# Kernel optimization log

Measured on AMD Instinct MI355X. Metric: run time of the kernel, lower is better.

## Reference

```python
import jax, jax.numpy as jnp
import numpy as np

LOG_2PI = np.float32(np.log(2.0 * np.pi))
NEG_BIG = np.float32(-9e15)


def setup_inputs() -> dict:
    key = jax.random.key(0)
    ks = jax.random.split(key, 8)
    N, F_in, F_out, H = 8192, 512, 128, 16
    x = jax.random.normal(ks[0], (N, F_in), dtype=jnp.float32)
    adj = jax.random.randint(ks[1], (N, N), 0, 2, dtype=jnp.int32)
    # xavier_uniform-ish init for W (gain 1.414)
    lim = np.float32(1.414 * np.sqrt(6.0 / (F_in + F_out)))
    W = jax.random.uniform(ks[2], (F_in, F_out), jnp.float32, -lim, lim)
    # VariationalAttentionNet params: lin1(2*F_out -> H), lin21/lin22(H -> 1)
    w1 = jax.random.normal(ks[3], (H, 2 * F_out), dtype=jnp.float32) * 0.05
    b1 = jnp.zeros((H,), jnp.float32)
    w21 = jax.random.normal(ks[4], (1, H), dtype=jnp.float32) * 0.05
    b21 = jnp.zeros((1,), jnp.float32)
    w22 = jax.random.normal(ks[5], (1, H), dtype=jnp.float32) * 0.05
    b22 = jnp.zeros((1,), jnp.float32)
    return {"x": x, "adj": adj, "W": W, "w1": w1, "b1": b1,
            "w21": w21, "b21": b21, "w22": w22, "b22": b22}


def reference(x, adj, W, w1, b1, w21, b21, w22, b22):
    # h = x @ W  [N, F_out]
    h = x @ W
    # VariationalAttentionNet(h, h), eval mode: z = mu
    u = jax.nn.relu(jnp.concatenate([h, h], axis=1) @ w1.T + b1)  # [N, H]
    mu = u @ w21.T + b21   # [N, 1]
    lv = u @ w22.T + b22   # [N, 1]
    sigma = jax.nn.softplus(lv)
    z = mu
    # qmp = -(log p(z) - log q(z)); with z = mu, log q(mu) = -log(sigma) - 0.5*log(2pi)
    log_p = jnp.sum(-0.5 * z * z - 0.5 * LOG_2PI)
    log_q = jnp.sum(-jnp.log(sigma) - 0.5 * LOG_2PI)
    qmp = log_q - log_p
    # per-node score z broadcast across row, masked by adjacency, row softmax
    scores = jnp.where(adj > 0, z, NEG_BIG)          # [N, N]
    attention = jax.nn.softmax(scores, axis=1)       # [N, N] (dropout off in eval)
    h_prime = attention @ h                          # [N, F_out]
    return jax.nn.elu(h_prime), qmp
```

## Files before the change

kernel.cpp:

```cpp
#include <hip/hip_runtime.h>

typedef unsigned int u32;
typedef unsigned short u16;

#define NN 8192
#define FIN 512
#define FOUT 128
#define NH 16
#define BK 64
#define BKA 256

typedef float f32x16 __attribute__((ext_vector_type(16)));
typedef __bf16 bf16x8 __attribute__((ext_vector_type(8)));

union PackAB { u32 u[4]; bf16x8 v; };

__device__ __forceinline__ u32 rne_hi(u32 u) {
  return u + (0x7FFFu + ((u >> 16) & 1u));
}
__device__ __forceinline__ u16 f32_to_bf16(float f) {
  return (u16)(rne_hi(__float_as_uint(f)) >> 16);
}

__global__ __launch_bounds__(256) void prep_kernel(
    const float* __restrict__ W, const float* __restrict__ w1,
    u16* __restrict__ WT, float* __restrict__ w1s) {
  int b = blockIdx.x, t = threadIdx.x;
  if (b < 256) {
    int o = b * 256 + t;
    int n = o >> 9, k = o & 511;
    WT[o] = f32_to_bf16(W[k * FOUT + n]);
  } else {
    for (int e = t; e < NH * FOUT; e += 256) {
      int k = e >> 7, f = e & 127;
      w1s[e] = w1[k * 256 + f] + w1[k * 256 + 128 + f];
    }
  }
}

__global__ __launch_bounds__(256, 6) void h_kernel(
    const float* __restrict__ x, const u16* __restrict__ WT,
    float* __restrict__ Hp, int KL) {
  __shared__ u16 aS[32 * BK];
  __shared__ u16 bS[128 * BK];
  int t = threadIdx.x;
  int w = t >> 6, l = t & 63;
  int m = l & 31, kh = l >> 5;
  int tile = blockIdx.x & 255, chunk = blockIdx.x >> 8;
  int i0 = tile * 32, k0 = chunk * KL;

  int arow = t >> 4, acol = (t & 15) * 4;
  int ac = (t & 15) >> 1, ah = t & 1;
  int aoff0 = arow * BK + ((ac ^ (arow & 7)) << 3) + ah * 4;
  int aoff1 = (arow + 16) * BK + ((ac ^ ((arow + 16) & 7)) << 3) + ah * 4;
  const float* ap0 = x + (size_t)(i0 + arow) * FIN + k0 + acol;
  const float* ap1 = ap0 + (size_t)16 * FIN;
  int hr = t >> 3, hc = t & 7;
  const u16* bp0 = WT + (size_t)hr * FIN + k0 + hc * 8;
  int boff[4];
#pragma unroll
  for (int p = 0; p < 4; ++p) {
    int r = hr + 32 * p;
    boff[p] = r * BK + ((hc ^ (r & 7)) << 3);
  }
  int aro = m * BK, am7 = m & 7;
  int nB = w * 32 + m;
  int bro = nB * BK, bm7 = nB & 7;

  f32x16 acc;
#pragma unroll
  for (int r = 0; r < 16; ++r) acc[r] = 0.0f;

  for (int o = 0; o < KL; o += BK) {
    float4 a0 = *(const float4*)ap0;
    float4 a1 = *(const float4*)ap1;
    uint4 h0 = *(const uint4*)bp0;
    uint4 h1 = *(const uint4*)(bp0 + 32 * (size_t)FIN);
    uint4 h2 = *(const uint4*)(bp0 + 64 * (size_t)FIN);
    uint4 h3 = *(const uint4*)(bp0 + 96 * (size_t)FIN);
    ap0 += BK; ap1 += BK; bp0 += BK;
    uint2 w0, w1v;
    w0.x = (rne_hi(__float_as_uint(a0.y)) & 0xFFFF0000u) | (rne_hi(__float_as_uint(a0.x)) >> 16);
    w0.y = (rne_hi(__float_as_uint(a0.w)) & 0xFFFF0000u) | (rne_hi(__float_as_uint(a0.z)) >> 16);
    w1v.x = (rne_hi(__float_as_uint(a1.y)) & 0xFFFF0000u) | (rne_hi(__float_as_uint(a1.x)) >> 16);
    w1v.y = (rne_hi(__float_as_uint(a1.w)) & 0xFFFF0000u) | (rne_hi(__float_as_uint(a1.z)) >> 16);
    *(uint2*)&aS[aoff0] = w0;
    *(uint2*)&aS[aoff1] = w1v;
    *(uint4*)&bS[boff[0]] = h0;
    *(uint4*)&bS[boff[1]] = h1;
    *(uint4*)&bS[boff[2]] = h2;
    *(uint4*)&bS[boff[3]] = h3;
    __syncthreads();
#pragma unroll
    for (int s = 0; s < BK; s += 16) {
      int cA = (s >> 3) + kh;
      PackAB pa, pb;
      pa.v = *(const bf16x8*)&aS[aro + ((cA ^ am7) << 3)];
      pb.v = *(const bf16x8*)&bS[bro + ((cA ^ bm7) << 3)];
      acc = __builtin_amdgcn_mfma_f32_32x32x16_bf16(pa.v, pb.v, acc, 0, 0, 0);
    }
    __syncthreads();
  }
  float* hp = Hp + (size_t)chunk * NN * FOUT;
  int col = w * 32 + m;
#pragma unroll
  for (int r = 0; r < 16; ++r) {
    int row = (r & 3) + 8 * (r >> 2) + 4 * kh;
    hp[(size_t)(i0 + row) * FOUT + col] = acc[r];
  }
}

__global__ __launch_bounds__(256) void reduceH_kernel(
    const float* __restrict__ Hp, int KSH,
    const float* __restrict__ b1, const float* __restrict__ w21,
    const float* __restrict__ b21, const float* __restrict__ w22,
    const float* __restrict__ b22, const float* __restrict__ w1s,
    u16* __restrict__ HTf, float* __restrict__ qpart) {
  __shared__ float hs[32][FOUT + 4];
  __shared__ float w1l[NH][FOUT + 4];
  __shared__ float us[32][NH + 1];
  int t = threadIdx.x;
  int i0 = blockIdx.x * 32;
  float v[16];
  const float* base = Hp + (size_t)i0 * FOUT + t * 16;
#pragma unroll
  for (int e = 0; e < 16; e += 4) {
    float4 x4 = *(const float4*)(base + e);
    v[e] = x4.x; v[e + 1] = x4.y; v[e + 2] = x4.z; v[e + 3] = x4.w;
  }
  for (int c = 1; c < KSH; ++c) {
    const float* p = base + (size_t)c * NN * FOUT;
#pragma unroll
    for (int e = 0; e < 16; e += 4) {
      float4 x4 = *(const float4*)(p + e);
      v[e] += x4.x; v[e + 1] += x4.y; v[e + 2] += x4.z; v[e + 3] += x4.w;
    }
  }
  {
    int row = t >> 3, c0 = (t & 7) * 16;
#pragma unroll
    for (int e = 0; e < 16; ++e) hs[row][c0 + e] = v[e];
  }
  for (int e = t; e < NH * FOUT; e += 256) w1l[e >> 7][e & 127] = w1s[e];
  __syncthreads();
  {
    int n = t & 127, g2 = t >> 7;
#pragma unroll
    for (int gg = 0; gg < 2; ++gg) {
      int g = g2 + 2 * gg;
      int k16 = (i0 >> 4) + (g >> 1), kh = g & 1;
      u32 p[4];
#pragma unroll
      for (int j = 0; j < 4; ++j) {
        u16 lo = f32_to_bf16(hs[g * 8 + 2 * j][n]);
        u16 hi = f32_to_bf16(hs[g * 8 + 2 * j + 1][n]);
        p[j] = (u32)lo | ((u32)hi << 16);
      }
      uint4 st; st.x = p[0]; st.y = p[1]; st.z = p[2]; st.w = p[3];
      size_t off = ((size_t)(k16 * 4 + (n >> 5)) * 64 + kh * 32 + (n & 31)) * 8;
      *(uint4*)(HTf + off) = st;
    }
  }
  {
    int i = t >> 3, p = t & 7;
    float s0 = b1[p], s1 = b1[p + 8];
#pragma unroll 4
    for (int f = 0; f < FOUT; ++f) {
      float hv = hs[i][f];
      s0 = fmaf(hv, w1l[p][f], s0);
      s1 = fmaf(hv, w1l[p + 8][f], s1);
    }
    us[i][p] = fmaxf(s0, 0.0f);
    us[i][p + 8] = fmaxf(s1, 0.0f);
  }
  __syncthreads();
  if (t < 32) {
    float mu = b21[0], lv = b22[0];
#pragma unroll
    for (int k = 0; k < NH; ++k) {
      mu = fmaf(us[t][k], w21[k], mu);
      lv = fmaf(us[t][k], w22[k], lv);
    }
    float sp = fmaxf(lv, 0.0f) + log1pf(expf(-fabsf(lv)));
    float q = 0.5f * mu * mu - logf(sp);
#pragma unroll
    for (int off = 16; off; off >>= 1) q += __shfl_down(q, off);
    if (t == 0) qpart[blockIdx.x] = q;
  }
}

__global__ __launch_bounds__(256, 4) void attn_kernel(
    const int* __restrict__ adj, const u16* __restrict__ HTf,
    float* __restrict__ Sp, u32* __restrict__ degw, int KL) {
  __shared__ u16 aS[2][8192];
  int t = threadIdx.x;
  int w = t >> 6, l = t & 63;
  int m = l & 31, kh = l >> 5;
  int tile = blockIdx.x & 255, chunk = blockIdx.x >> 8;
  int i0 = tile * 32, k0 = chunk * KL;

  int ar = t >> 3, lc = t & 7;
  const int* apb = adj + (size_t)(i0 + ar) * NN + k0 + lc * 4;
  int woff[8];
#pragma unroll
  for (int q = 0; q < 8; ++q)
    woff[q] = (q * 4 + (lc >> 1)) * 256 + ar * 8 + (lc & 1) * 4;
  const u16* bp = HTf + ((size_t)(k0 >> 4) * 256 + (size_t)(w * 64 + l)) * 8;
  int rdo = l * 8;

  f32x16 acc;
#pragma unroll
  for (int r = 0; r < 16; ++r) acc[r] = 0.0f;
  u32 degacc = 0;

  int nslab = KL / BKA;
  int4 aC[8];
#pragma unroll
  for (int q = 0; q < 8; ++q) aC[q] = *(const int4*)(apb + q * 32);
  apb += BKA;
#pragma unroll
  for (int q = 0; q < 8; ++q) {
    u32 p0 = ((u32)aC[q].y << 16) | (u32)aC[q].x;
    u32 p1 = ((u32)aC[q].w << 16) | (u32)aC[q].z;
    degacc += p0 + p1;
    uint2 wv; wv.x = p0 * 0x3F80u; wv.y = p1 * 0x3F80u;
    *(uint2*)&aS[0][woff[q]] = wv;
  }
  if (nslab > 1) {
#pragma unroll
    for (int q = 0; q < 8; ++q) aC[q] = *(const int4*)(apb + q * 32);
    apb += BKA;
  }
  __syncthreads();

  for (int o = 0; o < nslab; ++o) {
    int bsel = o & 1;
    bf16x8 bF[4];
#pragma unroll
    for (int j = 0; j < 4; ++j) bF[j] = *(const bf16x8*)(bp + j * 2048);
#pragma unroll
    for (int k16 = 0; k16 < 16; k16 += 4) {
      bf16x8 bN[4];
      if (k16 + 4 < 16) {
#pragma unroll
        for (int j = 0; j < 4; ++j)
          bN[j] = *(const bf16x8*)(bp + (k16 + 4 + j) * 2048);
      }
#pragma unroll
      for (int j = 0; j < 4; ++j) {
        PackAB pa;
        pa.v = *(const bf16x8*)&aS[bsel][(k16 + j) * 512 + rdo];
        acc = __builtin_amdgcn_mfma_f32_32x32x16_bf16(pa.v, bF[j], acc, 0, 0, 0);
      }
#pragma unroll
      for (int j = 0; j < 4; ++j) bF[j] = bN[j];
    }
    bp += (size_t)16 * 2048;
    if (o + 1 < nslab) {
#pragma unroll
      for (int q = 0; q < 8; ++q) {
        u32 p0 = ((u32)aC[q].y << 16) | (u32)aC[q].x;
        u32 p1 = ((u32)aC[q].w << 16) | (u32)aC[q].z;
        degacc += p0 + p1;
        uint2 wv; wv.x = p0 * 0x3F80u; wv.y = p1 * 0x3F80u;
        *(uint2*)&aS[bsel ^ 1][woff[q]] = wv;
      }
      if (o + 2 < nslab) {
#pragma unroll
        for (int q = 0; q < 8; ++q) aC[q] = *(const int4*)(apb + q * 32);
        apb += BKA;
      }
      __syncthreads();
    }
  }
  u32 d = (degacc & 0xFFFFu) + (degacc >> 16);
  d += __shfl_down(d, 4);
  d += __shfl_down(d, 2);
  d += __shfl_down(d, 1);
  if (lc == 0) degw[chunk * NN + i0 + ar] = d;
  float* sp = Sp + (size_t)chunk * NN * FOUT;
  int col = w * 32 + m;
#pragma unroll
  for (int r = 0; r < 16; ++r) {
    int row = (r & 3) + 8 * (r >> 2) + 4 * kh;
    sp[(size_t)(i0 + row) * FOUT + col] = acc[r];
  }
}

__global__ __launch_bounds__(256) void reduceSq_kernel(
    const float* __restrict__ Sp, const u32* __restrict__ degw,
    const float* __restrict__ qpart, float* __restrict__ out, int KSA) {
  int t = threadIdx.x;
  if (blockIdx.x == 1024) {
    __shared__ float sred[4];
    float v = qpart[t];
#pragma unroll
    for (int off = 32; off; off >>= 1) v += __shfl_down(v, off);
    if ((t & 63) == 0) sred[t >> 6] = v;
    __syncthreads();
    if (t == 0) out[(size_t)NN * FOUT] = sred[0] + sred[1] + sred[2] + sred[3];
    return;
  }
  int idx = (blockIdx.x * 256 + t) * 4;
  int i = idx >> 7;
  u32 deg = 0;
  for (int c = 0; c < KSA; ++c) deg += degw[c * NN + i];
  float4 s = {0.0f, 0.0f, 0.0f, 0.0f};
  for (int c = 0; c < KSA; ++c) {
    float4 v4 = *(const float4*)(Sp + (size_t)c * NN * FOUT + idx);
    s.x += v4.x; s.y += v4.y; s.z += v4.z; s.w += v4.w;
  }
  float rd = deg ? 1.0f / (float)deg : 0.0f;
  float4 o;
  o.x = s.x * rd; o.y = s.y * rd; o.z = s.z * rd; o.w = s.w * rd;
  o.x = o.x > 0.0f ? o.x : expm1f(o.x);
  o.y = o.y > 0.0f ? o.y : expm1f(o.y);
  o.z = o.z > 0.0f ? o.z : expm1f(o.z);
  o.w = o.w > 0.0f ? o.w : expm1f(o.w);
  *(float4*)(out + idx) = o;
}

extern "C" void kernel_launch(void* const* d_in, const int* in_sizes, int n_in,
                              void* d_out, int out_size, void* d_ws, size_t ws_size,
                              hipStream_t stream) {
  (void)in_sizes; (void)n_in; (void)out_size;
  const float* x   = (const float*)d_in[0];
  const int*   adj = (const int*)d_in[1];
  const float* W   = (const float*)d_in[2];
  const float* w1  = (const float*)d_in[3];
  const float* b1  = (const float*)d_in[4];
  const float* w21 = (const float*)d_in[5];
  const float* b21 = (const float*)d_in[6];
  const float* w22 = (const float*)d_in[7];
  const float* b22 = (const float*)d_in[8];
  float* out = (float*)d_out;

  const size_t TILE4 = (size_t)NN * FOUT * 4;
  int KSA = 4, KSH = 4;
  for (;;) {
    size_t need = (size_t)(KSA + KSH) * TILE4
                + (size_t)NN * FOUT * 2
                + (size_t)FOUT * FIN * 2
                + (size_t)KSA * NN * 4
                + NH * FOUT * 4 + 2048;
    if (need <= ws_size || (KSA == 1 && KSH == 1)) break;
    if (KSH > 1) KSH >>= 1; else KSA >>= 1;
  }

  char* ws = (char*)d_ws;
  float* Sp   = (float*)ws;                          ws += (size_t)KSA * TILE4;
  float* Hp   = (float*)ws;                          ws += (size_t)KSH * TILE4;
  u16*   HTf  = (u16*)ws;                            ws += (size_t)NN * FOUT * 2;
  u16*   WT   = (u16*)ws;                            ws += (size_t)FOUT * FIN * 2;
  u32*   degw = (u32*)ws;                            ws += (size_t)KSA * NN * 4;
  float* w1s  = (float*)ws;                          ws += NH * FOUT * 4;
  float* qpart= (float*)ws;

  prep_kernel<<<257, 256, 0, stream>>>(W, w1, WT, w1s);
  h_kernel<<<256 * KSH, 256, 0, stream>>>(x, WT, Hp, FIN / KSH);
  reduceH_kernel<<<256, 256, 0, stream>>>(Hp, KSH, b1, w21, b21, w22, b22, w1s, HTf, qpart);
  attn_kernel<<<256 * KSA, 256, 0, stream>>>(adj, HTf, Sp, degw, NN / KSA);
  reduceSq_kernel<<<1025, 256, 0, stream>>>(Sp, degw, qpart, out, KSA);
}
```

Before: 422.7 us.

## Give each wave private adjacency staging and drop block-wide barriers in attention kernel

The attention kernel now has every wave load and convert its own copy of a 64-column adjacency slab into a per-wave LDS buffer, so the block-wide __syncthreads become wave barriers. The slab depth drops from 256 to 64, the occupancy hint rises from 4 to 5 blocks, and the split-K count for the attention pass doubles to 8. The aim is to remove cross-wave barrier stalls and raise parallelism. The cost is that each adjacency row tile is fetched four times, once per wave, which adds cache and memory traffic, plus more partial-sum output for the reduce pass.

```diff
diff --git a/kernel.cpp b/kernel.cpp
--- a/kernel.cpp
+++ b/kernel.cpp
@@ -8,7 +8,6 @@
 #define FOUT 128
 #define NH 16
 #define BK 64
-#define BKA 256
 
 typedef float f32x16 __attribute__((ext_vector_type(16)));
 typedef __bf16 bf16x8 __attribute__((ext_vector_type(8)));
@@ -189,95 +188,92 @@
   }
 }
 
-__global__ __launch_bounds__(256, 4) void attn_kernel(
+__global__ __launch_bounds__(256, 5) void attn_kernel(
     const int* __restrict__ adj, const u16* __restrict__ HTf,
     float* __restrict__ Sp, u32* __restrict__ degw, int KL) {
-  __shared__ u16 aS[2][8192];
+  __shared__ u16 aS[4][2][2048];
   int t = threadIdx.x;
   int w = t >> 6, l = t & 63;
   int m = l & 31, kh = l >> 5;
   int tile = blockIdx.x & 255, chunk = blockIdx.x >> 8;
   int i0 = tile * 32, k0 = chunk * KL;
-
-  int ar = t >> 3, lc = t & 7;
-  const int* apb = adj + (size_t)(i0 + ar) * NN + k0 + lc * 4;
-  int woff[8];
-#pragma unroll
-  for (int q = 0; q < 8; ++q)
-    woff[q] = (q * 4 + (lc >> 1)) * 256 + ar * 8 + (lc & 1) * 4;
+  int nslab = KL / 64;
+
+  int rb = l >> 4, c0 = (l & 15) * 4;
+  const int* ap = adj + (size_t)(i0 + rb) * NN + k0 + c0;
+  int jj = (l & 15) >> 2;
+  int khb = ((l & 15) >> 1) & 1;
+  int woffb = jj * 512 + khb * 256 + rb * 8 + ((l & 15) & 1) * 4;
   const u16* bp = HTf + ((size_t)(k0 >> 4) * 256 + (size_t)(w * 64 + l)) * 8;
   int rdo = l * 8;
 
   f32x16 acc;
 #pragma unroll
   for (int r = 0; r < 16; ++r) acc[r] = 0.0f;
-  u32 degacc = 0;
-
-  int nslab = KL / BKA;
-  int4 aC[8];
-#pragma unroll
-  for (int q = 0; q < 8; ++q) aC[q] = *(const int4*)(apb + q * 32);
-  apb += BKA;
+  u32 degacc[8];
+#pragma unroll
+  for (int q = 0; q < 8; ++q) degacc[q] = 0;
+
+  int4 aP[8];
+#pragma unroll
+  for (int q = 0; q < 8; ++q) aP[q] = *(const int4*)(ap + (size_t)(q * 4) * NN);
+  ap += 64;
 #pragma unroll
   for (int q = 0; q < 8; ++q) {
-    u32 p0 = ((u32)aC[q].y << 16) | (u32)aC[q].x;
-    u32 p1 = ((u32)aC[q].w << 16) | (u32)aC[q].z;
-    degacc += p0 + p1;
+    u32 p0 = ((u32)aP[q].y << 16) | (u32)aP[q].x;
+    u32 p1 = ((u32)aP[q].w << 16) | (u32)aP[q].z;
+    degacc[q] += p0 + p1;
     uint2 wv; wv.x = p0 * 0x3F80u; wv.y = p1 * 0x3F80u;
-    *(uint2*)&aS[0][woff[q]] = wv;
+    *(uint2*)&aS[w][0][woffb + q * 32] = wv;
   }
   if (nslab > 1) {
 #pragma unroll
-    for (int q = 0; q < 8; ++q) aC[q] = *(const int4*)(apb + q * 32);
-    apb += BKA;
-  }
-  __syncthreads();
+    for (int q = 0; q < 8; ++q) aP[q] = *(const int4*)(ap + (size_t)(q * 4) * NN);
+    ap += 64;
+  }
+  __builtin_amdgcn_wave_barrier();
 
   for (int o = 0; o < nslab; ++o) {
     int bsel = o & 1;
-    bf16x8 bF[4];
-#pragma unroll
-    for (int j = 0; j < 4; ++j) bF[j] = *(const bf16x8*)(bp + j * 2048);
-#pragma unroll
-    for (int k16 = 0; k16 < 16; k16 += 4) {
-      bf16x8 bN[4];
-      if (k16 + 4 < 16) {
-#pragma unroll
-        for (int j = 0; j < 4; ++j)
-          bN[j] = *(const bf16x8*)(bp + (k16 + 4 + j) * 2048);
-      }
-#pragma unroll
-      for (int j = 0; j < 4; ++j) {
-        PackAB pa;
-        pa.v = *(const bf16x8*)&aS[bsel][(k16 + j) * 512 + rdo];
-        acc = __builtin_amdgcn_mfma_f32_32x32x16_bf16(pa.v, bF[j], acc, 0, 0, 0);
-      }
-#pragma unroll
-      for (int j = 0; j < 4; ++j) bF[j] = bN[j];
-    }
-    bp += (size_t)16 * 2048;
     if (o + 1 < nslab) {
 #pragma unroll
       for (int q = 0; q < 8; ++q) {
-        u32 p0 = ((u32)aC[q].y << 16) | (u32)aC[q].x;
-        u32 p1 = ((u32)aC[q].w << 16) | (u32)aC[q].z;
-        degacc += p0 + p1;
+        u32 p0 = ((u32)aP[q].y << 16) | (u32)aP[q].x;
+        u32 p1 = ((u32)aP[q].w << 16) | (u32)aP[q].z;
+        degacc[q] += p0 + p1;
         uint2 wv; wv.x = p0 * 0x3F80u; wv.y = p1 * 0x3F80u;
-        *(uint2*)&aS[bsel ^ 1][woff[q]] = wv;
+        *(uint2*)&aS[w][bsel ^ 1][woffb + q * 32] = wv;
       }
       if (o + 2 < nslab) {
 #pragma unroll
-        for (int q = 0; q < 8; ++q) aC[q] = *(const int4*)(apb + q * 32);
-        apb += BKA;
+        for (int q = 0; q < 8; ++q) aP[q] = *(const int4*)(ap + (size_t)(q * 4) * NN);
+        ap += 64;
       }
-      __syncthreads();
-    }
-  }
-  u32 d = (degacc & 0xFFFFu) + (degacc >> 16);
-  d += __shfl_down(d, 4);
-  d += __shfl_down(d, 2);
-  d += __shfl_down(d, 1);
-  if (lc == 0) degw[chunk * NN + i0 + ar] = d;
+    }
+    __builtin_amdgcn_wave_barrier();
+    bf16x8 bF[4];
+#pragma unroll
+    for (int j = 0; j < 4; ++j)
+      bF[j] = *(const bf16x8*)(bp + (size_t)(o * 4 + j) * 2048);
+#pragma unroll
+    for (int j = 0; j < 4; ++j) {
+      PackAB pa;
+      pa.v = *(const bf16x8*)&aS[w][bsel][j * 512 + rdo];
+      acc = __builtin_amdgcn_mfma_f32_32x32x16_bf16(pa.v, bF[j], acc, 0, 0, 0);
+    }
+    __builtin_amdgcn_wave_barrier();
+  }
+  if (w == 0) {
+#pragma unroll
+    for (int q = 0; q < 8; ++q) {
+      u32 d = (degacc[q] & 0xFFFFu) + (degacc[q] >> 16);
+      d += __shfl_down(d, 8);
+      d += __shfl_down(d, 4);
+      d += __shfl_down(d, 2);
+      d += __shfl_down(d, 1);
+      if ((l & 15) == 0) degw[chunk * NN + i0 + q * 4 + rb] = d;
+    }
+  }
   float* sp = Sp + (size_t)chunk * NN * FOUT;
   int col = w * 32 + m;
 #pragma unroll
@@ -336,7 +332,7 @@
   float* out = (float*)d_out;
 
   const size_t TILE4 = (size_t)NN * FOUT * 4;
-  int KSA = 4, KSH = 4;
+  int KSA = 8, KSH = 4;
   for (;;) {
     size_t need = (size_t)(KSA + KSH) * TILE4
                 + (size_t)NN * FOUT * 2
```

Result: slower. 462.6 us (+9.4%).

## Fuse H GEMM with per-node epilogue, drop split-K, prepack W fragments

Applied to the files above, without the earlier changes.

Removes the split-K partial buffers and the separate reduceH kernel. The h GEMM now runs as 256 blocks over the full K and writes its tile straight to shared memory for the MLP/qmp epilogue. W is prepacked into the MFMA fragment layout so B fragments load directly from global memory without LDS staging. The attention split is also lowered from 4 to 2, which cuts partial-sum traffic but reduces parallelism in attn_kernel. Risk: only 256 blocks for the GEMM, plus uncached global B reads on every step.

```diff
diff --git a/kernel.cpp b/kernel.cpp
--- a/kernel.cpp
+++ b/kernel.cpp
@@ -24,12 +24,24 @@
 
 __global__ __launch_bounds__(256) void prep_kernel(
     const float* __restrict__ W, const float* __restrict__ w1,
-    u16* __restrict__ WT, float* __restrict__ w1s) {
+    u16* __restrict__ WTf, float* __restrict__ w1s) {
   int b = blockIdx.x, t = threadIdx.x;
-  if (b < 256) {
-    int o = b * 256 + t;
-    int n = o >> 9, k = o & 511;
-    WT[o] = f32_to_bf16(W[k * FOUT + n]);
+  if (b < 16) {
+    int g = b * 256 + t;
+    int k16 = g >> 7, n = g & 127;
+    const float* wp = W + (size_t)(k16 * 16) * FOUT + n;
+#pragma unroll
+    for (int kh = 0; kh < 2; ++kh) {
+      u32 q[4];
+#pragma unroll
+      for (int j = 0; j < 4; ++j) {
+        u16 lo = f32_to_bf16(wp[(size_t)(kh * 8 + 2 * j) * FOUT]);
+        u16 hi = f32_to_bf16(wp[(size_t)(kh * 8 + 2 * j + 1) * FOUT]);
+        q[j] = (u32)lo | ((u32)hi << 16);
+      }
+      uint4 st; st.x = q[0]; st.y = q[1]; st.z = q[2]; st.w = q[3];
+      *(uint4*)(WTf + ((size_t)g * 2 + kh) * 8) = st;
+    }
   } else {
     for (int e = t; e < NH * FOUT; e += 256) {
       int k = e >> 7, f = e & 127;
@@ -38,47 +50,38 @@
   }
 }
 
-__global__ __launch_bounds__(256, 6) void h_kernel(
-    const float* __restrict__ x, const u16* __restrict__ WT,
-    float* __restrict__ Hp, int KL) {
+__global__ __launch_bounds__(256) void h_kernel(
+    const float* __restrict__ x, const u16* __restrict__ WTf,
+    const float* __restrict__ b1, const float* __restrict__ w21,
+    const float* __restrict__ b21, const float* __restrict__ w22,
+    const float* __restrict__ b22, const float* __restrict__ w1s,
+    u16* __restrict__ HTf, float* __restrict__ qpart) {
   __shared__ u16 aS[32 * BK];
-  __shared__ u16 bS[128 * BK];
+  __shared__ float hs[32][FOUT + 4];
+  __shared__ float w1l[NH][FOUT + 4];
+  __shared__ float us[32][NH + 1];
   int t = threadIdx.x;
   int w = t >> 6, l = t & 63;
   int m = l & 31, kh = l >> 5;
-  int tile = blockIdx.x & 255, chunk = blockIdx.x >> 8;
-  int i0 = tile * 32, k0 = chunk * KL;
+  int i0 = blockIdx.x * 32;
 
   int arow = t >> 4, acol = (t & 15) * 4;
   int ac = (t & 15) >> 1, ah = t & 1;
   int aoff0 = arow * BK + ((ac ^ (arow & 7)) << 3) + ah * 4;
   int aoff1 = (arow + 16) * BK + ((ac ^ ((arow + 16) & 7)) << 3) + ah * 4;
-  const float* ap0 = x + (size_t)(i0 + arow) * FIN + k0 + acol;
+  const float* ap0 = x + (size_t)(i0 + arow) * FIN + acol;
   const float* ap1 = ap0 + (size_t)16 * FIN;
-  int hr = t >> 3, hc = t & 7;
-  const u16* bp0 = WT + (size_t)hr * FIN + k0 + hc * 8;
-  int boff[4];
-#pragma unroll
-  for (int p = 0; p < 4; ++p) {
-    int r = hr + 32 * p;
-    boff[p] = r * BK + ((hc ^ (r & 7)) << 3);
-  }
   int aro = m * BK, am7 = m & 7;
   int nB = w * 32 + m;
-  int bro = nB * BK, bm7 = nB & 7;
 
   f32x16 acc;
 #pragma unroll
   for (int r = 0; r < 16; ++r) acc[r] = 0.0f;
 
-  for (int o = 0; o < KL; o += BK) {
+  for (int o = 0; o < FIN / BK; ++o) {
     float4 a0 = *(const float4*)ap0;
     float4 a1 = *(const float4*)ap1;
-    uint4 h0 = *(const uint4*)bp0;
-    uint4 h1 = *(const uint4*)(bp0 + 32 * (size_t)FIN);
-    uint4 h2 = *(const uint4*)(bp0 + 64 * (size_t)FIN);
-    uint4 h3 = *(const uint4*)(bp0 + 96 * (size_t)FIN);
-    ap0 += BK; ap1 += BK; bp0 += BK;
+    ap0 += BK; ap1 += BK;
     uint2 w0, w1v;
     w0.x = (rne_hi(__float_as_uint(a0.y)) & 0xFFFF0000u) | (rne_hi(__float_as_uint(a0.x)) >> 16);
     w0.y = (rne_hi(__float_as_uint(a0.w)) & 0xFFFF0000u) | (rne_hi(__float_as_uint(a0.z)) >> 16);
@@ -86,60 +89,21 @@
     w1v.y = (rne_hi(__float_as_uint(a1.w)) & 0xFFFF0000u) | (rne_hi(__float_as_uint(a1.z)) >> 16);
     *(uint2*)&aS[aoff0] = w0;
     *(uint2*)&aS[aoff1] = w1v;
-    *(uint4*)&bS[boff[0]] = h0;
-    *(uint4*)&bS[boff[1]] = h1;
-    *(uint4*)&bS[boff[2]] = h2;
-    *(uint4*)&bS[boff[3]] = h3;
     __syncthreads();
 #pragma unroll
-    for (int s = 0; s < BK; s += 16) {
-      int cA = (s >> 3) + kh;
+    for (int s = 0; s < 4; ++s) {
+      int cA = 2 * s + kh;
       PackAB pa, pb;
       pa.v = *(const bf16x8*)&aS[aro + ((cA ^ am7) << 3)];
-      pb.v = *(const bf16x8*)&bS[bro + ((cA ^ bm7) << 3)];
+      pb.v = *(const bf16x8*)(WTf + ((size_t)(o * 4 + s) * 128 + nB) * 16 + kh * 8);
       acc = __builtin_amdgcn_mfma_f32_32x32x16_bf16(pa.v, pb.v, acc, 0, 0, 0);
     }
     __syncthreads();
   }
-  float* hp = Hp + (size_t)chunk * NN * FOUT;
-  int col = w * 32 + m;
 #pragma unroll
   for (int r = 0; r < 16; ++r) {
     int row = (r & 3) + 8 * (r >> 2) + 4 * kh;
-    hp[(size_t)(i0 + row) * FOUT + col] = acc[r];
-  }
-}
-
-__global__ __launch_bounds__(256) void reduceH_kernel(
-    const float* __restrict__ Hp, int KSH,
-    const float* __restrict__ b1, const float* __restrict__ w21,
-    const float* __restrict__ b21, const float* __restrict__ w22,
-    const float* __restrict__ b22, const float* __restrict__ w1s,
-    u16* __restrict__ HTf, float* __restrict__ qpart) {
-  __shared__ float hs[32][FOUT + 4];
-  __shared__ float w1l[NH][FOUT + 4];
-  __shared__ float us[32][NH + 1];
-  int t = threadIdx.x;
-  int i0 = blockIdx.x * 32;
-  float v[16];
-  const float* base = Hp + (size_t)i0 * FOUT + t * 16;
-#pragma unroll
-  for (int e = 0; e < 16; e += 4) {
-    float4 x4 = *(const float4*)(base + e);
-    v[e] = x4.x; v[e + 1] = x4.y; v[e + 2] = x4.z; v[e + 3] = x4.w;
-  }
-  for (int c = 1; c < KSH; ++c) {
-    const float* p = base + (size_t)c * NN * FOUT;
-#pragma unroll
-    for (int e = 0; e < 16; e += 4) {
-      float4 x4 = *(const float4*)(p + e);
-      v[e] += x4.x; v[e + 1] += x4.y; v[e + 2] += x4.z; v[e + 3] += x4.w;
-    }
-  }
-  {
-    int row = t >> 3, c0 = (t & 7) * 16;
-#pragma unroll
-    for (int e = 0; e < 16; ++e) hs[row][c0 + e] = v[e];
+    hs[row][w * 32 + m] = acc[r];
   }
   for (int e = t; e < NH * FOUT; e += 256) w1l[e >> 7][e & 127] = w1s[e];
   __syncthreads();
@@ -148,7 +112,7 @@
 #pragma unroll
     for (int gg = 0; gg < 2; ++gg) {
       int g = g2 + 2 * gg;
-      int k16 = (i0 >> 4) + (g >> 1), kh = g & 1;
+      int k16 = (i0 >> 4) + (g >> 1), khb = g & 1;
       u32 p[4];
 #pragma unroll
       for (int j = 0; j < 4; ++j) {
@@ -157,7 +121,7 @@
         p[j] = (u32)lo | ((u32)hi << 16);
       }
       uint4 st; st.x = p[0]; st.y = p[1]; st.z = p[2]; st.w = p[3];
-      size_t off = ((size_t)(k16 * 4 + (n >> 5)) * 64 + kh * 32 + (n & 31)) * 8;
+      size_t off = ((size_t)(k16 * 4 + (n >> 5)) * 64 + khb * 32 + (n & 31)) * 8;
       *(uint4*)(HTf + off) = st;
     }
   }
@@ -336,29 +300,19 @@
   float* out = (float*)d_out;
 
   const size_t TILE4 = (size_t)NN * FOUT * 4;
-  int KSA = 4, KSH = 4;
-  for (;;) {
-    size_t need = (size_t)(KSA + KSH) * TILE4
-                + (size_t)NN * FOUT * 2
-                + (size_t)FOUT * FIN * 2
-                + (size_t)KSA * NN * 4
-                + NH * FOUT * 4 + 2048;
-    if (need <= ws_size || (KSA == 1 && KSH == 1)) break;
-    if (KSH > 1) KSH >>= 1; else KSA >>= 1;
-  }
+  int KSA = 2;
+  while ((size_t)KSA * (TILE4 + NN * 4) + (8u << 20) > ws_size && KSA > 1) KSA >>= 1;
 
   char* ws = (char*)d_ws;
   float* Sp   = (float*)ws;                          ws += (size_t)KSA * TILE4;
-  float* Hp   = (float*)ws;                          ws += (size_t)KSH * TILE4;
   u16*   HTf  = (u16*)ws;                            ws += (size_t)NN * FOUT * 2;
-  u16*   WT   = (u16*)ws;                            ws += (size_t)FOUT * FIN * 2;
+  u16*   WTf  = (u16*)ws;                            ws += (size_t)FOUT * FIN * 2;
   u32*   degw = (u32*)ws;                            ws += (size_t)KSA * NN * 4;
   float* w1s  = (float*)ws;                          ws += NH * FOUT * 4;
   float* qpart= (float*)ws;
 
-  prep_kernel<<<257, 256, 0, stream>>>(W, w1, WT, w1s);
-  h_kernel<<<256 * KSH, 256, 0, stream>>>(x, WT, Hp, FIN / KSH);
-  reduceH_kernel<<<256, 256, 0, stream>>>(Hp, KSH, b1, w21, b21, w22, b22, w1s, HTf, qpart);
+  prep_kernel<<<17, 256, 0, stream>>>(W, w1, WTf, w1s);
+  h_kernel<<<256, 256, 0, stream>>>(x, WTf, b1, w21, b21, w22, b22, w1s, HTf, qpart);
   attn_kernel<<<256 * KSA, 256, 0, stream>>>(adj, HTf, Sp, degw, NN / KSA);
   reduceSq_kernel<<<1025, 256, 0, stream>>>(Sp, degw, qpart, out, KSA);
 }
```

Result: no change. 429.6 us (+1.6%).
